# Performance work log

Hardware: AMD Instinct MI355X
Metric: run time of the kernel (lower is better)

Reference implementation:

```python
import jax, jax.numpy as jnp
import numpy as np

B = 8192      # batch (nodes)
HOPS = 15
SEQ = HOPS + 1
IN = 512      # input_dim
H = 256       # hidden_dim
DS = 64       # d_state
L = 6         # n_layers
NC = 40       # n_class
EPS = 1e-5


def _ln(x, g, b):
    m = x.mean(-1, keepdims=True)
    v = x.var(-1, keepdims=True)  # population var, matches torch LayerNorm
    return (x - m) / jnp.sqrt(v + EPS) * g + b


def setup_inputs() -> dict:
    key = jax.random.key(0)
    ks = jax.random.split(key, 16)
    n = lambda k, shp: jax.random.normal(k, shp, dtype=jnp.float32) * 0.02
    inp = {}
    inp["batched_data"] = jax.random.normal(ks[0], (B, SEQ, IN), dtype=jnp.float32)
    inp["in_w"] = n(ks[1], (H, IN)); inp["in_b"] = jnp.zeros((H,), jnp.float32)
    # per-layer stacked params (leading dim L); note: each MambaBlock shares ONE
    # LayerNorm instance for both pre-ssm and pre-ffn norm.
    inp["norm_g"] = jnp.ones((L, H), jnp.float32); inp["norm_b"] = jnp.zeros((L, H), jnp.float32)
    inp["A_w"] = n(ks[2], (L, DS, H))
    inp["B_w"] = n(ks[3], (L, DS, H))
    inp["C_w"] = n(ks[4], (L, H, DS))
    inp["D_w"] = n(ks[5], (L, H, H)); inp["D_b"] = jnp.zeros((L, H), jnp.float32)
    inp["gate_w"] = n(ks[6], (L, H, H)); inp["gate_b"] = jnp.zeros((L, H), jnp.float32)
    inp["ffn_w1"] = n(ks[7], (L, 2 * H, H)); inp["ffn_b1"] = jnp.zeros((L, 2 * H), jnp.float32)
    inp["ffn_w2"] = n(ks[8], (L, H, 2 * H)); inp["ffn_b2"] = jnp.zeros((L, H), jnp.float32)
    inp["fln_g"] = jnp.ones((H,), jnp.float32); inp["fln_b"] = jnp.zeros((H,), jnp.float32)
    inp["out_w"] = n(ks[9], (H // 2, H)); inp["out_b"] = jnp.zeros((H // 2,), jnp.float32)
    inp["cls_w"] = n(ks[10], (NC, H // 2)); inp["cls_b"] = jnp.zeros((NC,), jnp.float32)
    inp["attn_w"] = n(ks[11], (1, 2 * H)); inp["attn_b"] = jnp.zeros((1,), jnp.float32)
    return inp


def reference(batched_data, in_w, in_b, norm_g, norm_b, A_w, B_w, C_w, D_w, D_b,
              gate_w, gate_b, ffn_w1, ffn_b1, ffn_w2, ffn_b2, fln_g, fln_b,
              out_w, out_b, cls_w, cls_b, attn_w, attn_b):
    x = batched_data @ in_w.T + in_b  # [B,S,H]

    def layer(x, p):
        ng, nb, Aw, Bw, Cw, Dw, Db, gw, gb, w1, b1, w2, b2 = p
        y = _ln(x, ng, nb)
        # precompute all per-step projections in batched GEMMs
        a = jnp.tanh(jnp.einsum('bsh,dh->bsd', y, Aw))   # [B,S,DS]
        bt = jnp.einsum('bsh,dh->bsd', y, Bw)            # [B,S,DS]
        g = jax.nn.sigmoid(y @ gw.T + gb)                # [B,S,H]
        dt = y @ Dw.T + Db                               # [B,S,H]

        def step(h, ab):
            at, bbt = ab
            h = at * h + bbt
            return h, h

        h0 = jnp.zeros((x.shape[0], Aw.shape[0]), x.dtype)
        _, hs = jax.lax.scan(step, h0, (a.transpose(1, 0, 2), bt.transpose(1, 0, 2)))  # [S,B,DS]
        ys = jnp.einsum('sbd,hd->bsh', hs, Cw)           # [B,S,H]
        x = x + ys * g + dt * (1.0 - g)
        y = _ln(x, ng, nb)  # same norm params (shared LayerNorm in block)
        y = jax.nn.gelu(y @ w1.T + b1, approximate=False) @ w2.T + b2
        return x + y, None

    x, _ = jax.lax.scan(layer, x, (norm_g, norm_b, A_w, B_w, C_w, D_w, D_b,
                                   gate_w, gate_b, ffn_w1, ffn_b1, ffn_w2, ffn_b2))
    x = _ln(x, fln_g, fln_b)
    node = x[:, :1, :]           # [B,1,H]
    nbr = x[:, 1:, :]            # [B,S-1,H]
    ai = jnp.concatenate([jnp.broadcast_to(node, nbr.shape), nbr], axis=2)  # [B,S-1,2H]
    aw = jax.nn.softmax(ai @ attn_w.T + attn_b, axis=1)  # [B,S-1,1]
    agg = jnp.sum(nbr * aw, axis=1, keepdims=True)
    out = (node + agg)[:, 0, :]
    out = jax.nn.relu(out @ out_w.T + out_b) @ cls_w.T + cls_b
    return jax.nn.log_softmax(out, axis=1)
```

## Files before the change

### kernel.cpp

```cpp
#include <hip/hip_runtime.h>

typedef __attribute__((ext_vector_type(8))) short bf16x8_t;
typedef __attribute__((ext_vector_type(4))) float f32x4_t;

__device__ __forceinline__ ushort f2bf(float x) {
  union { float f; unsigned u; } a; a.f = x;
  unsigned r = a.u + 0x7fffu + ((a.u >> 16) & 1u);
  return (ushort)(r >> 16);
}
__device__ __forceinline__ float bf2f(ushort s) {
  union { unsigned u; float f; } a; a.u = ((unsigned)s) << 16;
  return a.f;
}
__device__ __forceinline__ void gload_lds16(const void* g, void* l) {
  __builtin_amdgcn_global_load_lds(
      (const __attribute__((address_space(1))) unsigned int*)g,
      (__attribute__((address_space(3))) unsigned int*)l, 16, 0, 0);
}
__device__ __forceinline__ int swzkey(int r) { return ((r >> 2) ^ r) & 3; }

__global__ void cvt_kernel(const float* __restrict__ s, ushort* __restrict__ d, int n) {
  int i = blockIdx.x * 256 + threadIdx.x;
  if (i < n) d[i] = f2bf(s[i]);
}

__global__ void cvt4_kernel(const float* __restrict__ s, ushort* __restrict__ d, long n4) {
  long i = (long)blockIdx.x * 256 + threadIdx.x;
  if (i < n4) {
    float4 v = ((const float4*)s)[i];
    ushort4 o;
    o.x = f2bf(v.x); o.y = f2bf(v.y); o.z = f2bf(v.z); o.w = f2bf(v.w);
    ((ushort4*)d)[i] = o;
  }
}

__global__ void build_wcat(const float* __restrict__ Aw, const float* __restrict__ Bw,
                           const float* __restrict__ gw, const float* __restrict__ Dw,
                           ushort* __restrict__ out) {
  int i = blockIdx.x * 256 + threadIdx.x;
  if (i >= 6 * 640 * 256) return;
  int l = i / (640 * 256), r = (i / 256) % 640, c = i % 256;
  float v;
  if (r < 64)        v = Aw[((l * 64 + r) * 256) + c];
  else if (r < 128)  v = Bw[((l * 64 + (r - 64)) * 256) + c];
  else if (r < 384)  v = gw[((l * 256 + (r - 128)) * 256) + c];
  else               v = Dw[((l * 256 + (r - 384)) * 256) + c];
  out[i] = f2bf(v);
}

__global__ void repack_gen(const ushort* __restrict__ src, ushort* __restrict__ dst,
                           int K, int perMat, int dstPerMat, int dstOff, long total) {
  const long i = (long)blockIdx.x * 256 + threadIdx.x;
  if (i >= total) return;
  const int m = (int)(i / perMat);
  const int idx = (int)(i % perMat);
  const int slice = idx >> 12;
  const int ksn = K >> 5;
  const int p = slice / ksn, ks = slice - p * ksn;
  const int r = (idx >> 5) & 127;
  const int s = (idx >> 3) & 3;
  const int e = idx & 7;
  const int k = ks * 32 + ((s ^ ((r >> 1) & 3)) << 3) + e;
  dst[(long)m * dstPerMat + dstOff + idx] = src[(long)m * perMat + (p * 128 + r) * K + k];
}

__global__ __launch_bounds__(256, 4)
void mamba_fused(ushort* __restrict__ y, ushort* __restrict__ xP,
                 const ushort* __restrict__ Wk,
                 const float* __restrict__ gb, const float* __restrict__ db,
                 const float* __restrict__ lng, const float* __restrict__ lnb) {
  __shared__ __align__(16) char WsB[16384];
  __shared__ __align__(16) ushort ab[32 * 136];
  __shared__ __align__(16) char HsB[4096];
  __shared__ float lsum[32][2], lsq[32][2];

  const int t = threadIdx.x, lane = t & 63, wid = t >> 6;
  const long m0 = (long)blockIdx.x * 32;
  const int wr = (wid >> 1) * 16, wc = (wid & 1) * 64;
  const int co = wid * 2;
  const char* Wb = (const char*)Wk;

  const int krow = lane & 15, kslot = lane >> 4;
  const int ar = wr + krow;

  bf16x8_t afr[8];
  {
    const char* yrow = (const char*)y + (m0 + ar) * 512 + kslot * 16;
#pragma unroll
    for (int ks = 0; ks < 8; ++ks) afr[ks] = *(const bf16x8_t*)(yrow + ks * 64);
  }
  gload_lds16(Wb + co * 1024 + lane * 16, WsB + co * 1024);
  gload_lds16(Wb + (co + 1) * 1024 + lane * 16, WsB + (co + 1) * 1024);

  int boff[4];
#pragma unroll
  for (int i = 0; i < 4; ++i) {
    const int br = wc + i * 16 + krow;
    boff[i] = br * 64 + ((kslot ^ ((br >> 1) & 3)) << 4);
  }
  const int rbase = (lane >> 4) * 4, cbase = lane & 15;

  const f32x4_t zero = {0.f, 0.f, 0.f, 0.f};
  f32x4_t acc[4];
#pragma unroll
  for (int i = 0; i < 4; ++i) acc[i] = zero;

  int tau = 0;
  auto kstep = [&](bf16x8_t af) {
    __syncthreads();
    if (tau + 1 < 44) {
      const char* src = Wb + (long)(tau + 1) * 8192;
      char* dst = WsB + ((tau + 1) & 1) * 8192;
      gload_lds16(src + co * 1024 + lane * 16, dst + co * 1024);
      gload_lds16(src + (co + 1) * 1024 + lane * 16, dst + (co + 1) * 1024);
    }
    const char* Wc = WsB + (tau & 1) * 8192;
    bf16x8_t bv[4];
#pragma unroll
    for (int i = 0; i < 4; ++i) bv[i] = *(const bf16x8_t*)(Wc + boff[i]);
    __builtin_amdgcn_s_setprio(1);
#pragma unroll
    for (int ni = 0; ni < 4; ++ni)
      acc[ni] = __builtin_amdgcn_mfma_f32_16x16x32_bf16(af, bv[ni], acc[ni], 0, 0, 0);
    __builtin_amdgcn_s_setprio(0);
    ++tau;
  };

#pragma unroll
  for (int ks = 0; ks < 8; ++ks) kstep(afr[ks]);
#pragma unroll
  for (int ni = 0; ni < 4; ++ni) {
    const int col = wc + ni * 16 + cbase;
#pragma unroll
    for (int j = 0; j < 4; ++j) {
      const int row = wr + rbase + j;
      const float v = acc[ni][j];
      ab[row * 136 + col] = f2bf(col < 64 ? tanhf(v) : v);
    }
    acc[ni] = zero;
  }
  __syncthreads();
  if (t < 128) {
    const int b = t >> 6, d = t & 63;
    float av[16], btv[16];
#pragma unroll
    for (int s = 0; s < 16; ++s) {
      const int row = b * 16 + s;
      av[s]  = bf2f(ab[row * 136 + d]);
      btv[s] = bf2f(ab[row * 136 + 64 + d]);
    }
    float h = 0.f;
#pragma unroll
    for (int s = 0; s < 16; ++s) {
      h = fmaf(av[s], h, btv[s]);
      const int row = b * 16 + s;
      *(ushort*)(HsB + row * 128 + (((d >> 3) ^ (row & 7)) << 4) + (d & 7) * 2) = f2bf(h);
    }
  }

  f32x4_t gsv[2][4], dsv[2][4], xnv[2][4];
#pragma unroll
  for (int pp = 0; pp < 2; ++pp) {
#pragma unroll
    for (int ks = 0; ks < 8; ++ks) kstep(afr[ks]);
#pragma unroll
    for (int ni = 0; ni < 4; ++ni) {
      const int col = pp * 128 + wc + ni * 16 + cbase;
#pragma unroll
      for (int j = 0; j < 4; ++j) {
        const float s = acc[ni][j] + gb[col];
        gsv[pp][ni][j] = 1.f / (1.f + expf(-s));
      }
      acc[ni] = zero;
    }
  }
#pragma unroll
  for (int pp = 0; pp < 2; ++pp) {
#pragma unroll
    for (int ks = 0; ks < 8; ++ks) kstep(afr[ks]);
#pragma unroll
    for (int ni = 0; ni < 4; ++ni) {
      const int col = pp * 128 + wc + ni * 16 + cbase;
#pragma unroll
      for (int j = 0; j < 4; ++j) dsv[pp][ni][j] = acc[ni][j] + db[col];
      acc[ni] = zero;
    }
  }
  const long rq16 = (m0 >> 4) + (wr >> 4);
#pragma unroll
  for (int pp = 0; pp < 2; ++pp) {
#pragma unroll
    for (int ks = 0; ks < 2; ++ks) {
      const bf16x8_t afh = *(const bf16x8_t*)(
          HsB + (ar << 7) + ((((ks << 2) | kslot) ^ (ar & 7)) << 4));
      kstep(afh);
    }
#pragma unroll
    for (int ni = 0; ni < 4; ++ni) {
      const int colq = pp * 8 + (wid & 1) * 4 + ni;
      const ushort4 x4 = *(const ushort4*)(xP + (rq16 * 16 + colq) * 256 + lane * 4);
#pragma unroll
      for (int j = 0; j < 4; ++j) {
        const float g = gsv[pp][ni][j], dv = dsv[pp][ni][j];
        const float xo = bf2f(j == 0 ? x4.x : (j == 1 ? x4.y : (j == 2 ? x4.z : x4.w)));
        xnv[pp][ni][j] = xo + acc[ni][j] * g + dv * (1.f - g);
      }
      acc[ni] = zero;
    }
  }
#pragma unroll
  for (int j = 0; j < 4; ++j) {
    float ps = 0.f, pq = 0.f;
#pragma unroll
    for (int pp = 0; pp < 2; ++pp)
#pragma unroll
      for (int ni = 0; ni < 4; ++ni) { const float v = xnv[pp][ni][j]; ps += v; pq += v * v; }
#pragma unroll
    for (int off = 1; off < 16; off <<= 1) {
      ps += __shfl_xor(ps, off, 64);
      pq += __shfl_xor(pq, off, 64);
    }
    if ((lane & 15) == 0) {
      const int row = wr + rbase + j;
      lsum[row][wid & 1] = ps;
      lsq[row][wid & 1] = pq;
    }
  }
  __syncthreads();
#pragma unroll
  for (int pp = 0; pp < 2; ++pp) {
#pragma unroll
    for (int ni = 0; ni < 4; ++ni) {
      const int colq = pp * 8 + (wid & 1) * 4 + ni;
      ushort4 o4;
      o4.x = f2bf(xnv[pp][ni][0]);
      o4.y = f2bf(xnv[pp][ni][1]);
      o4.z = f2bf(xnv[pp][ni][2]);
      o4.w = f2bf(xnv[pp][ni][3]);
      *(ushort4*)(xP + (rq16 * 16 + colq) * 256 + lane * 4) = o4;
    }
  }
#pragma unroll
  for (int j = 0; j < 4; ++j) {
    const int row = wr + rbase + j;
    const float sm = lsum[row][0] + lsum[row][1];
    const float q = lsq[row][0] + lsq[row][1];
    const float mean = sm * (1.f / 256.f);
    const float rstd = rsqrtf(q * (1.f / 256.f) - mean * mean + 1e-5f);
#pragma unroll
    for (int pp = 0; pp < 2; ++pp)
#pragma unroll
      for (int ni = 0; ni < 4; ++ni) {
        const int col = pp * 128 + wc + ni * 16 + cbase;
        *(ushort*)(WsB + row * 512 + col * 2) =
            f2bf((xnv[pp][ni][j] - mean) * rstd * lng[col] + lnb[col]);
      }
  }
  __syncthreads();
#pragma unroll
  for (int rr = 0; rr < 4; ++rr) {
    const int byte = rr * 4096 + t * 16;
    const int row = byte >> 9, off = byte & 511;
    const bf16x8_t v = *(const bf16x8_t*)(WsB + byte);
    *(bf16x8_t*)((char*)y + (m0 + row) * 512 + off) = v;
  }
}

template <int NP, int MODE>
__global__ __launch_bounds__(256, 2)
void gemm_ws(const ushort* __restrict__ A, const ushort* __restrict__ Wks,
             const float* __restrict__ b1, ushort* __restrict__ outp) {
  constexpr int KS = 8;
  constexpr int N = NP * 128;
  constexpr int T = NP * KS;
  __shared__ __align__(16) char AsB[128 * 512];
  __shared__ __align__(16) char WsB[2 * 8192];

  const int t = threadIdx.x, lane = t & 63, wid = t >> 6;
  const long m0 = (long)blockIdx.x * 128;
  const int wr = (wid >> 1) * 64, wc = (wid & 1) * 64;
  const char* Ab = (const char*)A;
  const char* Wb = (const char*)Wks;

  {
    const int arow = lane >> 5;
    const int aps  = lane & 31;
#pragma unroll
    for (int j = 0; j < 16; ++j) {
      const int r = j * 8 + wid * 2 + arow;
      gload_lds16(Ab + (m0 + r) * 512 + (long)((aps ^ (r & 7)) << 4),
                  AsB + (j * 8 + wid * 2) * 512);
    }
  }
  {
    const int co = wid * 2;
    gload_lds16(Wb + co * 1024 + lane * 16, WsB + co * 1024);
    gload_lds16(Wb + (co + 1) * 1024 + lane * 16, WsB + (co + 1) * 1024);
  }

  const int krow = lane & 15, kslot = lane >> 4;
  int abase[4], akey[4], boff[4];
#pragma unroll
  for (int i = 0; i < 4; ++i) {
    const int ar = wr + i * 16 + krow;
    abase[i] = ar * 512;
    akey[i] = ar & 7;
    const int br = wc + i * 16 + krow;
    boff[i] = br * 64 + ((kslot ^ ((br >> 1) & 3)) << 4);
  }

  const f32x4_t zero = {0.f, 0.f, 0.f, 0.f};
  f32x4_t acc[4][4];
#pragma unroll
  for (int i = 0; i < 4; ++i)
#pragma unroll
    for (int j = 0; j < 4; ++j) acc[i][j] = zero;

  const int rbase = (lane >> 4) * 4, cbase = lane & 15;

  for (int tau = 0; tau < T; ++tau) {
    __syncthreads();
    if (tau + 1 < T) {
      const int co = wid * 2;
      char* dst = WsB + ((tau + 1) & 1) * 8192;
      const char* src = Wb + (long)(tau + 1) * 8192;
      gload_lds16(src + co * 1024 + lane * 16, dst + co * 1024);
      gload_lds16(src + (co + 1) * 1024 + lane * 16, dst + (co + 1) * 1024);
    }
    const int ks = tau & 7;
    const char* Wc = WsB + (tau & 1) * 8192;
    bf16x8_t af[4], bv[4];
#pragma unroll
    for (int i = 0; i < 4; ++i)
      af[i] = *(const bf16x8_t*)(AsB + abase[i] + ((((ks << 2) | kslot) ^ akey[i]) << 4));
#pragma unroll
    for (int i = 0; i < 4; ++i) bv[i] = *(const bf16x8_t*)(Wc + boff[i]);
    __builtin_amdgcn_s_setprio(1);
#pragma unroll
    for (int mi = 0; mi < 4; ++mi)
#pragma unroll
      for (int ni = 0; ni < 4; ++ni)
        acc[mi][ni] = __builtin_amdgcn_mfma_f32_16x16x32_bf16(af[mi], bv[ni], acc[mi][ni], 0, 0, 0);
    __builtin_amdgcn_s_setprio(0);

    if (ks == KS - 1) {
      const int np = tau >> 3;
#pragma unroll
      for (int mi = 0; mi < 4; ++mi) {
#pragma unroll
        for (int ni = 0; ni < 4; ++ni) {
          const int col = np * 128 + wc + ni * 16 + cbase;
#pragma unroll
          for (int j = 0; j < 4; ++j) {
            const long row = m0 + wr + mi * 16 + rbase + j;
            float s = acc[mi][ni][j] + b1[col];
            float o = 0.5f * s * (1.f + erff(s * 0.70710678118654752f));
            outp[row * N + col] = f2bf(o);
          }
          acc[mi][ni] = zero;
        }
      }
    }
  }
}

template <int K, int MODE>
__global__ __launch_bounds__(512)
void gemm_ln(const ushort* __restrict__ A, const ushort* __restrict__ W,
             const float* __restrict__ b1, ushort* __restrict__ xP,
             const float* __restrict__ lng, const float* __restrict__ lnb,
             ushort* __restrict__ y, int writex) {
  constexpr int KS = K / 32;
  __shared__ __align__(16) char WsB[2 * 16384];
  __shared__ __align__(16) char AsB[2 * 8192];
  __shared__ float lsum4[128][4], lsq4[128][4];

  const int t = threadIdx.x, lane = t & 63, wid = t >> 6;
  const int wr = (wid >> 2) * 64, wc = (wid & 3) * 64;
  const int lr = lane >> 2, lc = lane & 3;
  const int ra = wid * 16 + lr;
  const int saA = (lc ^ swzkey(ra)) << 4;
  const int rw0 = wid * 32 + lr, rw1 = rw0 + 16;
  const int sw0 = (lc ^ swzkey(rw0)) << 4;
  const int sw1 = (lc ^ swzkey(rw1)) << 4;
  const char* Ab = (const char*)A;
  const char* Wb = (const char*)W;
  constexpr long K2 = (long)K * 2;
  const long m0 = (long)blockIdx.x * 128;

  gload_lds16(Wb + (long)rw0 * K2 + sw0, WsB + wid * 2048);
  gload_lds16(Wb + (long)rw1 * K2 + sw1, WsB + wid * 2048 + 1024);
  gload_lds16(Ab + (m0 + ra) * K2 + saA, AsB + wid * 1024);

  const int krow = lane & 15, kslot = lane >> 4;
  int aoff[4], boff[4];
#pragma unroll
  for (int i = 0; i < 4; ++i) {
    int ar = wr + i * 16 + krow;
    aoff[i] = ar * 64 + ((kslot ^ swzkey(ar)) << 4);
    int br = wc + i * 16 + krow;
    boff[i] = br * 64 + ((kslot ^ swzkey(br)) << 4);
  }

  const f32x4_t zero = {0.f, 0.f, 0.f, 0.f};
  f32x4_t acc[4][4];
#pragma unroll
  for (int i = 0; i < 4; ++i)
#pragma unroll
    for (int j = 0; j < 4; ++j) acc[i][j] = zero;

  for (int tau = 0; tau < KS; ++tau) {
    __syncthreads();
    if (tau + 1 < KS) {
      const long kb = (long)(tau + 1) * 64;
      gload_lds16(Ab + (m0 + ra) * K2 + kb + saA, AsB + ((tau + 1) & 1) * 8192 + wid * 1024);
      char* wd = WsB + ((tau + 1) & 1) * 16384 + wid * 2048;
      gload_lds16(Wb + (long)rw0 * K2 + kb + sw0, wd);
      gload_lds16(Wb + (long)rw1 * K2 + kb + sw1, wd + 1024);
    }
    const char* Ac = AsB + (tau & 1) * 8192;
    const char* Wc = WsB + (tau & 1) * 16384;
    bf16x8_t af[4], bv[4];
#pragma unroll
    for (int i = 0; i < 4; ++i) af[i] = *(const bf16x8_t*)(Ac + aoff[i]);
#pragma unroll
    for (int i = 0; i < 4; ++i) bv[i] = *(const bf16x8_t*)(Wc + boff[i]);
#pragma unroll
    for (int mi = 0; mi < 4; ++mi)
#pragma unroll
      for (int ni = 0; ni < 4; ++ni)
        acc[mi][ni] = __builtin_amdgcn_mfma_f32_16x16x32_bf16(af[mi], bv[ni], acc[mi][ni], 0, 0, 0);
  }

  const int rbase = (lane >> 4) * 4;
  const int cbase = lane & 15;
  const long xbB = (long)blockIdx.x * 32768;
#pragma unroll
  for (int mi = 0; mi < 4; ++mi) {
    const int rq = (wid >> 2) * 4 + mi;
#pragma unroll
    for (int ni = 0; ni < 4; ++ni) {
      const int col = wc + ni * 16 + cbase;
      const int cq = (wid & 3) * 4 + ni;
      ushort4 x4;
      if constexpr (MODE == 3) x4 = *(const ushort4*)(xP + xbB + ((rq * 16 + cq) * 64 + lane) * 4);
#pragma unroll
      for (int j = 0; j < 4; ++j) {
        float v = acc[mi][ni][j] + b1[col];
        if constexpr (MODE == 3)
          v += bf2f(j == 0 ? x4.x : (j == 1 ? x4.y : (j == 2 ? x4.z : x4.w)));
        acc[mi][ni][j] = v;
      }
    }
  }
#pragma unroll
  for (int mi = 0; mi < 4; ++mi) {
#pragma unroll
    for (int j = 0; j < 4; ++j) {
      float ps = 0.f, pq = 0.f;
#pragma unroll
      for (int ni = 0; ni < 4; ++ni) { float v = acc[mi][ni][j]; ps += v; pq += v * v; }
#pragma unroll
      for (int off = 1; off < 16; off <<= 1) {
        ps += __shfl_xor(ps, off, 64);
        pq += __shfl_xor(pq, off, 64);
      }
      if ((lane & 15) == 0) {
        int r = wr + mi * 16 + (lane >> 4) * 4 + j;
        lsum4[r][wid & 3] = ps;
        lsq4[r][wid & 3] = pq;
      }
    }
  }
  __syncthreads();
#pragma unroll
  for (int mi = 0; mi < 4; ++mi) {
    const int rq = (wid >> 2) * 4 + mi;
#pragma unroll
    for (int ni = 0; ni < 4; ++ni) {
      const int cq = (wid & 3) * 4 + ni;
      if (writex) {
        ushort4 o4;
        o4.x = f2bf(acc[mi][ni][0]);
        o4.y = f2bf(acc[mi][ni][1]);
        o4.z = f2bf(acc[mi][ni][2]);
        o4.w = f2bf(acc[mi][ni][3]);
        *(ushort4*)(xP + xbB + ((rq * 16 + cq) * 64 + lane) * 4) = o4;
      }
    }
  }
#pragma unroll
  for (int mi = 0; mi < 4; ++mi) {
#pragma unroll
    for (int j = 0; j < 4; ++j) {
      const int r = wr + mi * 16 + rbase + j;
      const float s = lsum4[r][0] + lsum4[r][1] + lsum4[r][2] + lsum4[r][3];
      const float q = lsq4[r][0] + lsq4[r][1] + lsq4[r][2] + lsq4[r][3];
      const float mean = s * (1.f / 256.f);
      const float rstd = rsqrtf(q * (1.f / 256.f) - mean * mean + 1e-5f);
      const long row = m0 + r;
#pragma unroll
      for (int ni = 0; ni < 4; ++ni) {
        const int col = wc + ni * 16 + cbase;
        y[row * 256 + col] = f2bf((acc[mi][ni][j] - mean) * rstd * lng[col] + lnb[col]);
      }
    }
  }
}

__global__ __launch_bounds__(256)
void head_kernel(const ushort* __restrict__ yin, const float* __restrict__ attw,
                 const float* __restrict__ ow, const float* __restrict__ ob,
                 const float* __restrict__ cw, const float* __restrict__ cb,
                 float* __restrict__ out) {
  __shared__ float xf[16][256];
  __shared__ float lg[16], aw[16];
  __shared__ float vs[256], o1[128], lgc[40], lse[1];
  const int t = threadIdx.x, lane = t & 63, wid = t >> 6;
  const ushort* yb = yin + (long)blockIdx.x * 16 * 256;

  for (int r = wid; r < 16; r += 4) {
    ushort4 u = *(const ushort4*)(yb + r * 256 + lane * 4);
    int c = lane * 4;
    xf[r][c + 0] = bf2f(u.x);
    xf[r][c + 1] = bf2f(u.y);
    xf[r][c + 2] = bf2f(u.z);
    xf[r][c + 3] = bf2f(u.w);
  }
  __syncthreads();

  for (int r = wid; r < 16; r += 4) {
    const float* wv = attw + (r == 0 ? 0 : 256);
    int c = lane * 4;
    float s = xf[r][c] * wv[c] + xf[r][c + 1] * wv[c + 1] +
              xf[r][c + 2] * wv[c + 2] + xf[r][c + 3] * wv[c + 3];
#pragma unroll
    for (int off = 32; off > 0; off >>= 1) s += __shfl_xor(s, off, 64);
    if (lane == 0) lg[r] = s;
  }
  __syncthreads();

  if (t == 0) {
    float mx = -1e30f;
    for (int s2 = 1; s2 < 16; ++s2) mx = fmaxf(mx, lg[s2]);
    float den = 0.f;
    for (int s2 = 1; s2 < 16; ++s2) { float e = expf(lg[s2] - mx); aw[s2] = e; den += e; }
    float inv = 1.f / den;
    for (int s2 = 1; s2 < 16; ++s2) aw[s2] *= inv;
  }
  __syncthreads();

  float vh = xf[0][t];
  for (int s2 = 1; s2 < 16; ++s2) vh += aw[s2] * xf[s2][t];
  vs[t] = vh;
  __syncthreads();

  if (t < 128) {
    float s = ob[t];
    const float* w = ow + t * 256;
    for (int h2 = 0; h2 < 256; ++h2) s += w[h2] * vs[h2];
    o1[t] = fmaxf(s, 0.f);
  }
  __syncthreads();

  if (t < 40) {
    float s = cb[t];
    const float* w = cw + t * 128;
    for (int j = 0; j < 128; ++j) s += w[j] * o1[j];
    lgc[t] = s;
  }
  __syncthreads();

  if (t == 0) {
    float mx = -1e30f;
    for (int c2 = 0; c2 < 40; ++c2) mx = fmaxf(mx, lgc[c2]);
    float den = 0.f;
    for (int c2 = 0; c2 < 40; ++c2) den += expf(lgc[c2] - mx);
    lse[0] = mx + logf(den);
  }
  __syncthreads();
  if (t < 40) out[(long)blockIdx.x * 40 + t] = lgc[t] - lse[0];
}

extern "C" void kernel_launch(void* const* d_in, const int* in_sizes, int n_in,
                              void* d_out, int out_size, void* d_ws, size_t ws_size,
                              hipStream_t stream) {
  const float* data   = (const float*)d_in[0];
  const float* in_w   = (const float*)d_in[1];
  const float* in_b   = (const float*)d_in[2];
  const float* norm_g = (const float*)d_in[3];
  const float* norm_b = (const float*)d_in[4];
  const float* A_w    = (const float*)d_in[5];
  const float* B_w    = (const float*)d_in[6];
  const float* C_w    = (const float*)d_in[7];
  const float* D_w    = (const float*)d_in[8];
  const float* D_b    = (const float*)d_in[9];
  const float* gate_w = (const float*)d_in[10];
  const float* gate_b = (const float*)d_in[11];
  const float* ffn_w1 = (const float*)d_in[12];
  const float* ffn_b1 = (const float*)d_in[13];
  const float* ffn_w2 = (const float*)d_in[14];
  const float* ffn_b2 = (const float*)d_in[15];
  const float* fln_g  = (const float*)d_in[16];
  const float* fln_b  = (const float*)d_in[17];
  const float* out_w  = (const float*)d_in[18];
  const float* out_b  = (const float*)d_in[19];
  const float* cls_w  = (const float*)d_in[20];
  const float* cls_b  = (const float*)d_in[21];
  const float* attn_w = (const float*)d_in[22];
  const float* attn_b = (const float*)d_in[23];
  (void)in_sizes; (void)n_in; (void)out_size; (void)ws_size; (void)attn_b;

  char* ws = (char*)d_ws;
  ushort* xP     = (ushort*)(ws + 0);
  ushort* y      = (ushort*)(ws + 67108864);
  ushort* tzp    = (ushort*)(ws + 134217728);
  ushort* wcat   = (ushort*)(ws + 318767104);
  ushort* inwb   = (ushort*)(ws + 320733184);
  ushort* w1b    = (ushort*)(ws + 320995328);
  ushort* w2b    = (ushort*)(ws + 322568192);
  ushort* cwb    = (ushort*)(ws + 324141056);
  ushort* mslice = (ushort*)(ws + 324337664);
  ushort* w1k    = (ushort*)(ws + 326500352);
  ushort* datab  = tzp;

  cvt_kernel<<<512, 256, 0, stream>>>(in_w, inwb, 131072);
  cvt_kernel<<<3072, 256, 0, stream>>>(ffn_w1, w1b, 786432);
  cvt_kernel<<<3072, 256, 0, stream>>>(ffn_w2, w2b, 786432);
  cvt_kernel<<<384, 256, 0, stream>>>(C_w, cwb, 98304);
  build_wcat<<<3840, 256, 0, stream>>>(A_w, B_w, gate_w, D_w, wcat);
  repack_gen<<<3840, 256, 0, stream>>>(wcat, mslice, 256, 163840, 180224, 0, 6L * 163840);
  repack_gen<<<384, 256, 0, stream>>>(cwb, mslice, 64, 16384, 180224, 163840, 6L * 16384);
  repack_gen<<<3072, 256, 0, stream>>>(w1b, w1k, 256, 131072, 131072, 0, 6L * 131072);
  cvt4_kernel<<<65536, 256, 0, stream>>>(data, datab, 16777216);

  gemm_ln<512, 0><<<dim3(1024), 512, 0, stream>>>(
      datab, inwb, in_b, xP, norm_g, norm_b, y, 1);

  for (int l = 0; l < 6; ++l) {
    mamba_fused<<<4096, 256, 0, stream>>>(
        y, xP, mslice + (size_t)l * 180224,
        gate_b + l * 256, D_b + l * 256, norm_g + l * 256, norm_b + l * 256);
    gemm_ws<4, 2><<<1024, 256, 0, stream>>>(
        y, w1k + (size_t)l * 131072, ffn_b1 + l * 512, tzp);
    const float* lg2 = (l < 5) ? (norm_g + (l + 1) * 256) : fln_g;
    const float* lb2 = (l < 5) ? (norm_b + (l + 1) * 256) : fln_b;
    gemm_ln<512, 3><<<dim3(1024), 512, 0, stream>>>(
        tzp, w2b + (size_t)l * 256 * 512, ffn_b2 + l * 256, xP, lg2, lb2, y, (l < 5) ? 1 : 0);
  }

  head_kernel<<<8192, 256, 0, stream>>>(y, attn_w, out_w, out_b, cls_w, cls_b, (float*)d_out);
}
```

Baseline: 2.381 ms.

## Split head into wave-per-node aggregation, MFMA out-projection GEMM, and classifier kernel

Replaces the one-block-per-node head kernel with three stages. A wave-per-node attention aggregation kernel keeps all rows in registers and uses shuffle reductions. The 256→128 output projection with ReLU now runs as a bf16 MFMA GEMM (gemm_ws in a new ReLU mode) on a repacked copy of out_w. A wave-per-node classifier then computes log-softmax. This removes the scalar per-thread matvecs and heavy syncthreads use of the old head, at the cost of extra launches, bf16 rounding of the intermediate activations, and a few small weight conversion kernels.

```diff
diff --git a/kernel.cpp b/kernel.cpp
--- a/kernel.cpp
+++ b/kernel.cpp
@@ -354,7 +354,9 @@
           for (int j = 0; j < 4; ++j) {
             const long row = m0 + wr + mi * 16 + rbase + j;
             float s = acc[mi][ni][j] + b1[col];
-            float o = 0.5f * s * (1.f + erff(s * 0.70710678118654752f));
+            float o;
+            if constexpr (MODE == 2) o = 0.5f * s * (1.f + erff(s * 0.70710678118654752f));
+            else                     o = fmaxf(s, 0.f);
             outp[row * N + col] = f2bf(o);
           }
           acc[mi][ni] = zero;
@@ -509,77 +511,73 @@
 }
 
 __global__ __launch_bounds__(256)
-void head_kernel(const ushort* __restrict__ yin, const float* __restrict__ attw,
-                 const float* __restrict__ ow, const float* __restrict__ ob,
-                 const float* __restrict__ cw, const float* __restrict__ cb,
-                 float* __restrict__ out) {
-  __shared__ float xf[16][256];
-  __shared__ float lg[16], aw[16];
-  __shared__ float vs[256], o1[128], lgc[40], lse[1];
-  const int t = threadIdx.x, lane = t & 63, wid = t >> 6;
-  const ushort* yb = yin + (long)blockIdx.x * 16 * 256;
-
-  for (int r = wid; r < 16; r += 4) {
-    ushort4 u = *(const ushort4*)(yb + r * 256 + lane * 4);
-    int c = lane * 4;
-    xf[r][c + 0] = bf2f(u.x);
-    xf[r][c + 1] = bf2f(u.y);
-    xf[r][c + 2] = bf2f(u.z);
-    xf[r][c + 3] = bf2f(u.w);
-  }
-  __syncthreads();
-
-  for (int r = wid; r < 16; r += 4) {
-    const float* wv = attw + (r == 0 ? 0 : 256);
-    int c = lane * 4;
-    float s = xf[r][c] * wv[c] + xf[r][c + 1] * wv[c + 1] +
-              xf[r][c + 2] * wv[c + 2] + xf[r][c + 3] * wv[c + 3];
-#pragma unroll
-    for (int off = 32; off > 0; off >>= 1) s += __shfl_xor(s, off, 64);
-    if (lane == 0) lg[r] = s;
-  }
-  __syncthreads();
-
-  if (t == 0) {
-    float mx = -1e30f;
-    for (int s2 = 1; s2 < 16; ++s2) mx = fmaxf(mx, lg[s2]);
-    float den = 0.f;
-    for (int s2 = 1; s2 < 16; ++s2) { float e = expf(lg[s2] - mx); aw[s2] = e; den += e; }
-    float inv = 1.f / den;
-    for (int s2 = 1; s2 < 16; ++s2) aw[s2] *= inv;
-  }
-  __syncthreads();
-
-  float vh = xf[0][t];
-  for (int s2 = 1; s2 < 16; ++s2) vh += aw[s2] * xf[s2][t];
-  vs[t] = vh;
-  __syncthreads();
-
-  if (t < 128) {
-    float s = ob[t];
-    const float* w = ow + t * 256;
-    for (int h2 = 0; h2 < 256; ++h2) s += w[h2] * vs[h2];
-    o1[t] = fmaxf(s, 0.f);
-  }
-  __syncthreads();
-
-  if (t < 40) {
-    float s = cb[t];
-    const float* w = cw + t * 128;
-    for (int j = 0; j < 128; ++j) s += w[j] * o1[j];
-    lgc[t] = s;
-  }
-  __syncthreads();
-
-  if (t == 0) {
-    float mx = -1e30f;
-    for (int c2 = 0; c2 < 40; ++c2) mx = fmaxf(mx, lgc[c2]);
-    float den = 0.f;
-    for (int c2 = 0; c2 < 40; ++c2) den += expf(lgc[c2] - mx);
-    lse[0] = mx + logf(den);
-  }
-  __syncthreads();
-  if (t < 40) out[(long)blockIdx.x * 40 + t] = lgc[t] - lse[0];
+void head_agg(const ushort* __restrict__ y, const float* __restrict__ attw,
+              ushort* __restrict__ vb) {
+  const int t = threadIdx.x, lane = t & 63, w = t >> 6;
+  const long b = (long)blockIdx.x * 4 + w;
+  const ushort* yb = y + b * 16 * 256;
+  const float4 w2 = *(const float4*)(attw + 256 + lane * 4);
+
+  float4 rows[16];
+  float lg[16];
+#pragma unroll
+  for (int r = 0; r < 16; ++r) {
+    const ushort4 u = *(const ushort4*)(yb + r * 256 + lane * 4);
+    float4 v4;
+    v4.x = bf2f(u.x); v4.y = bf2f(u.y); v4.z = bf2f(u.z); v4.w = bf2f(u.w);
+    rows[r] = v4;
+    if (r >= 1) {
+      float s = v4.x * w2.x + v4.y * w2.y + v4.z * w2.z + v4.w * w2.w;
+#pragma unroll
+      for (int off = 32; off > 0; off >>= 1) s += __shfl_xor(s, off, 64);
+      lg[r] = s;
+    }
+  }
+  float mx = -1e30f;
+#pragma unroll
+  for (int r = 1; r < 16; ++r) mx = fmaxf(mx, lg[r]);
+  float den = 0.f;
+#pragma unroll
+  for (int r = 1; r < 16; ++r) { lg[r] = expf(lg[r] - mx); den += lg[r]; }
+  const float inv = 1.f / den;
+  float4 v = rows[0];
+#pragma unroll
+  for (int r = 1; r < 16; ++r) {
+    const float a = lg[r] * inv;
+    v.x += a * rows[r].x; v.y += a * rows[r].y;
+    v.z += a * rows[r].z; v.w += a * rows[r].w;
+  }
+  ushort4 o;
+  o.x = f2bf(v.x); o.y = f2bf(v.y); o.z = f2bf(v.z); o.w = f2bf(v.w);
+  *(ushort4*)(vb + b * 256 + lane * 4) = o;
+}
+
+__global__ __launch_bounds__(256)
+void head_cls(const ushort* __restrict__ o1b, const float* __restrict__ cw,
+              const float* __restrict__ cb, float* __restrict__ out) {
+  __shared__ float lw[4][40];
+  const int t = threadIdx.x, lane = t & 63, w = t >> 6;
+  const long b = (long)blockIdx.x * 4 + w;
+  const ushort2 u = *(const ushort2*)(o1b + b * 128 + lane * 2);
+  const float o1x = bf2f(u.x), o1y = bf2f(u.y);
+
+#pragma unroll
+  for (int o = 0; o < 40; ++o) {
+    const float2 c = *(const float2*)(cw + o * 128 + lane * 2);
+    float p = o1x * c.x + o1y * c.y;
+#pragma unroll
+    for (int off = 32; off > 0; off >>= 1) p += __shfl_xor(p, off, 64);
+    if (lane == 0) lw[w][o] = p + cb[o];
+  }
+  const float v = (lane < 40) ? lw[w][lane] : -1e30f;
+  float mx = v;
+#pragma unroll
+  for (int off = 32; off > 0; off >>= 1) mx = fmaxf(mx, __shfl_xor(mx, off, 64));
+  float e = (lane < 40) ? expf(v - mx) : 0.f;
+  float den = e;
+#pragma unroll
+  for (int off = 32; off > 0; off >>= 1) den += __shfl_xor(den, off, 64);
+  if (lane < 40) out[b * 40 + lane] = v - mx - logf(den);
 }
 
 extern "C" void kernel_launch(void* const* d_in, const int* in_sizes, int n_in,
@@ -622,16 +620,22 @@
   ushort* cwb    = (ushort*)(ws + 324141056);
   ushort* mslice = (ushort*)(ws + 324337664);
   ushort* w1k    = (ushort*)(ws + 326500352);
+  ushort* owb    = (ushort*)(ws + 328073216);
+  ushort* owk    = (ushort*)(ws + 328138752);
   ushort* datab  = tzp;
+  ushort* vb     = tzp;
+  ushort* o1b    = tzp + 2097152;
 
   cvt_kernel<<<512, 256, 0, stream>>>(in_w, inwb, 131072);
   cvt_kernel<<<3072, 256, 0, stream>>>(ffn_w1, w1b, 786432);
   cvt_kernel<<<3072, 256, 0, stream>>>(ffn_w2, w2b, 786432);
   cvt_kernel<<<384, 256, 0, stream>>>(C_w, cwb, 98304);
+  cvt_kernel<<<128, 256, 0, stream>>>(out_w, owb, 32768);
   build_wcat<<<3840, 256, 0, stream>>>(A_w, B_w, gate_w, D_w, wcat);
   repack_gen<<<3840, 256, 0, stream>>>(wcat, mslice, 256, 163840, 180224, 0, 6L * 163840);
   repack_gen<<<384, 256, 0, stream>>>(cwb, mslice, 64, 16384, 180224, 163840, 6L * 16384);
   repack_gen<<<3072, 256, 0, stream>>>(w1b, w1k, 256, 131072, 131072, 0, 6L * 131072);
+  repack_gen<<<128, 256, 0, stream>>>(owb, owk, 256, 32768, 32768, 0, 32768);
   cvt4_kernel<<<65536, 256, 0, stream>>>(data, datab, 16777216);
 
   gemm_ln<512, 0><<<dim3(1024), 512, 0, stream>>>(
@@ -649,5 +653,7 @@
         tzp, w2b + (size_t)l * 256 * 512, ffn_b2 + l * 256, xP, lg2, lb2, y, (l < 5) ? 1 : 0);
   }
 
-  head_kernel<<<8192, 256, 0, stream>>>(y, attn_w, out_w, out_b, cls_w, cls_b, (float*)d_out);
-}
+  head_agg<<<2048, 256, 0, stream>>>(y, attn_w, vb);
+  gemm_ws<1, 3><<<64, 256, 0, stream>>>(vb, owk, out_b, o1b);
+  head_cls<<<2048, 256, 0, stream>>>(o1b, cls_w, cls_b, (float*)d_out);
+}
```

Measured after the change: 2.295 ms. -3.6%, faster.
